# Performance work log

Measured on AMD Instinct MI355X. Metric: run time of the kernel, lower is better.

## Reference

```python
import jax, jax.numpy as jnp
import numpy as np

N = 50000      # nodes
F_IN = 500     # in_channels
MID = 64       # mid_layer_channel
H = 2          # heads
OUT = 40       # out_channels
E = 800000     # edges per order
ORDER = 3
NEG_SLOPE = 0.2


def _gat(x, edge_index, W, a_src, a_dst, b, concat):
    # PyG-style GATConv (eval mode, dropout off), with self loops.
    n = x.shape[0]
    heads, ch = a_src.shape
    h = (x @ W).reshape(n, heads, ch)                    # [N,H,C]
    loop = jnp.arange(n)
    src = jnp.concatenate([edge_index[0], loop])
    dst = jnp.concatenate([edge_index[1], loop])
    al_s = jnp.sum(h * a_src, axis=-1)                   # [N,H]
    al_d = jnp.sum(h * a_dst, axis=-1)                   # [N,H]
    e = jax.nn.leaky_relu(al_s[src] + al_d[dst], NEG_SLOPE)   # [Etot,H]
    m = jax.ops.segment_max(e, dst, num_segments=n)      # softmax over incoming edges per dst
    ex = jnp.exp(e - m[dst])
    den = jax.ops.segment_sum(ex, dst, num_segments=n)
    alpha = ex / (den[dst] + 1e-16)
    out = jax.ops.segment_sum(alpha[:, :, None] * h[src], dst, num_segments=n)  # [N,H,C]
    if concat:
        return out.reshape(n, heads * ch) + b
    return out.mean(axis=1) + b


def _aggr(states, Wmix, wfin):
    # NOrderAggrConv (depth=2): mix order states with [order,order] weights + ELU,
    # then reduce to a single state with a learned [order] combination.
    h = jnp.stack(states, axis=1)                        # [N,order,C]
    h = jax.nn.elu(jnp.einsum('nkc,kj->njc', h, Wmix))
    return jnp.einsum('nkc,k->nc', h, wfin)


def setup_inputs():
    key = jax.random.key(0)
    ks = jax.random.split(key, 40)
    d = {}
    d['node_feature'] = jax.random.normal(ks[0], (N, F_IN), jnp.float32)
    for o in range(ORDER):
        d[f'adj{o}'] = jax.random.randint(ks[1 + o], (2, E), 0, N)
    i = 4
    s = 0.05
    layer_dims = [(F_IN, MID, H * MID), (MID * H, OUT, OUT)]
    for l, (fin, c, bdim) in enumerate(layer_dims):
        for o in range(ORDER):
            d[f'W_{l}_{o}'] = jax.random.normal(ks[i], (fin, H * c), jnp.float32) * s; i += 1
            d[f'as_{l}_{o}'] = jax.random.normal(ks[i], (H, c), jnp.float32) * s; i += 1
            d[f'ad_{l}_{o}'] = jax.random.normal(ks[i], (H, c), jnp.float32) * s; i += 1
            d[f'b_{l}_{o}'] = jnp.zeros((bdim,), jnp.float32)
    for l in range(2):
        d[f'agg{l}_W'] = jax.random.normal(ks[i], (ORDER, ORDER), jnp.float32) * 0.5; i += 1
        d[f'agg{l}_w'] = jnp.full((ORDER,), 1.0 / ORDER, jnp.float32)
    return d


def reference(node_feature, adj0, adj1, adj2,
              W_0_0, as_0_0, ad_0_0, b_0_0,
              W_0_1, as_0_1, ad_0_1, b_0_1,
              W_0_2, as_0_2, ad_0_2, b_0_2,
              W_1_0, as_1_0, ad_1_0, b_1_0,
              W_1_1, as_1_1, ad_1_1, b_1_1,
              W_1_2, as_1_2, ad_1_2, b_1_2,
              agg0_W, agg0_w, agg1_W, agg1_w):
    adjs = (adj0, adj1, adj2)
    p0 = ((W_0_0, as_0_0, ad_0_0, b_0_0),
          (W_0_1, as_0_1, ad_0_1, b_0_1),
          (W_0_2, as_0_2, ad_0_2, b_0_2))
    p1 = ((W_1_0, as_1_0, ad_1_0, b_1_0),
          (W_1_1, as_1_1, ad_1_1, b_1_1),
          (W_1_2, as_1_2, ad_1_2, b_1_2))
    aggs = ((agg0_W, agg0_w), (agg1_W, agg1_w))
    x = node_feature  # eval mode: dropout is identity
    for l, params in enumerate((p0, p1)):
        concat = (l == 0)
        states = [jax.nn.elu(_gat(x, adjs[o], *params[o], concat)) for o in range(ORDER)]
        x = _aggr(states, *aggs[l])
    return jax.nn.log_softmax(x, axis=1)
```

## Files before the change

### kernel.cpp

```cpp
#include <hip/hip_runtime.h>
#include <cstdint>
#include <cstddef>
#include <math.h>


typedef __attribute__((ext_vector_type(8))) short short8;
typedef __attribute__((ext_vector_type(4))) float f32x4;
typedef __attribute__((ext_vector_type(2))) float f32x2;

struct P3f { const float* p[3]; };
struct P3c { const int* p[3]; };

__device__ __forceinline__ float leakyf(float x) { return x > 0.f ? x : 0.2f * x; }
__device__ __forceinline__ float eluf(float x)   { return x > 0.f ? x : expm1f(x); }

__device__ __forceinline__ unsigned short bf16r(float x) {
  unsigned int u = __float_as_uint(x);
  u += 0x7fffu + ((u >> 16) & 1u);
  return (unsigned short)(u >> 16);
}
__device__ __forceinline__ float bflo(unsigned int u) { return __uint_as_float(u << 16); }
__device__ __forceinline__ float bfhi(unsigned int u) { return __uint_as_float(u & 0xffff0000u); }

__device__ __forceinline__ void bf8_fma2(uint4 q, float xx, f32x2* a) {
  f32x2 v0 = {bflo(q.x), bfhi(q.x)};
  f32x2 v1 = {bflo(q.y), bfhi(q.y)};
  f32x2 v2 = {bflo(q.z), bfhi(q.z)};
  f32x2 v3 = {bflo(q.w), bfhi(q.w)};
  a[0] += xx * v0;
  a[1] += xx * v1;
  a[2] += xx * v2;
  a[3] += xx * v3;
}

__global__ __launch_bounds__(256) void zero_int_kernel(int* p, int n) {
  int i = blockIdx.x * blockDim.x + threadIdx.x;
  if (i < n) p[i] = 0;
}

__global__ __launch_bounds__(256) void convA_kernel(const float* __restrict__ A,
    unsigned short* __restrict__ Ab, int M, int K, int Kpad) {
  int i = blockIdx.x * blockDim.x + threadIdx.x;
  int row = i >> 6;
  int koff = (i & 63) * 8;
  if (row >= M) return;
  const float* ap = A + (size_t)row * K;
  unsigned short v[8];
  if (koff + 8 <= K) {
    float4 q0 = ((const float4*)(ap + koff))[0];
    float4 q1 = ((const float4*)(ap + koff))[1];
    v[0] = bf16r(q0.x); v[1] = bf16r(q0.y); v[2] = bf16r(q0.z); v[3] = bf16r(q0.w);
    v[4] = bf16r(q1.x); v[5] = bf16r(q1.y); v[6] = bf16r(q1.z); v[7] = bf16r(q1.w);
  } else {
#pragma unroll
    for (int k = 0; k < 8; ++k)
      v[k] = (koff + k < K) ? bf16r(ap[koff + k]) : (unsigned short)0;
  }
  *(uint4*)(Ab + (size_t)row * Kpad + koff) = *(const uint4*)v;
}

__global__ __launch_bounds__(256) void count3_kernel(P3c adj, int* __restrict__ cntb,
                                                     int E, int N) {
  int i = blockIdx.x * blockDim.x + threadIdx.x;
  int o = blockIdx.y;
  if (i < E) atomicAdd(&cntb[o * N + adj.p[o][E + i]], 1);
}

#define SCAN_T 256
#define SCAN_VPT 8
#define SCAN_TILE 2048

__global__ __launch_bounds__(SCAN_T) void scan1_kernel(const int* __restrict__ cntb,
    int* __restrict__ rowptrb, int* __restrict__ bsums, int N) {
  __shared__ int lds[SCAN_T];
  const int o = blockIdx.y;
  const int* cnt = cntb + o * N;
  int* rowptr = rowptrb + o * (N + 1);
  int t = threadIdx.x;
  int base = blockIdx.x * SCAN_TILE + t * SCAN_VPT;
  int v[SCAN_VPT];
  int s = 0;
#pragma unroll
  for (int i = 0; i < SCAN_VPT; ++i) {
    int idx = base + i;
    int x = (idx < N) ? cnt[idx] : 0;
    s += x;
    v[i] = s;
  }
  lds[t] = s;
  __syncthreads();
  for (int off = 1; off < SCAN_T; off <<= 1) {
    int add = (t >= off) ? lds[t - off] : 0;
    __syncthreads();
    lds[t] += add;
    __syncthreads();
  }
  int excl = (t > 0) ? lds[t - 1] : 0;
#pragma unroll
  for (int i = 0; i < SCAN_VPT; ++i) {
    int idx = base + i;
    if (idx < N) rowptr[idx + 1] = excl + v[i];
  }
  if (t == SCAN_T - 1) bsums[o * 64 + blockIdx.x] = lds[t];
}

__global__ void scan2_kernel(int* bsums, int nb, int* rowptrb, int N) {
  if (threadIdx.x == 0 && blockIdx.x == 0) {
    for (int o = 0; o < 3; ++o) {
      int run = 0;
      for (int i = 0; i < nb; ++i) {
        int x = bsums[o * 64 + i];
        bsums[o * 64 + i] = run;
        run += x;
      }
      rowptrb[o * (N + 1)] = 0;
    }
  }
}

__global__ __launch_bounds__(256) void scan3_kernel(int* __restrict__ rowptrb,
    const int* __restrict__ bsums, int N) {
  int idx = blockIdx.x * blockDim.x + threadIdx.x;
  int o = blockIdx.y;
  if (idx < N) rowptrb[o * (N + 1) + idx + 1] += bsums[o * 64 + idx / SCAN_TILE];
}

__global__ __launch_bounds__(256) void fill3_kernel(P3c adj,
    const int* __restrict__ rowptrb, int* __restrict__ curb,
    int* __restrict__ colvb, int E, int N) {
  int i = blockIdx.x * blockDim.x + threadIdx.x;
  int o = blockIdx.y;
  if (i < E) {
    const int* a = adj.p[o];
    int d = a[E + i];
    int pos = atomicAdd(&curb[o * N + d], 1);
    colvb[(size_t)o * E + rowptrb[o * (N + 1) + d] + pos] = a[i];
  }
}

__global__ __launch_bounds__(256) void conv_bt3_kernel(P3f W,
    unsigned short* __restrict__ BtB, int K, int NC, int Kpad) {
  int n = blockIdx.y;
  int o = blockIdx.z;
  int k = blockIdx.x * 256 + threadIdx.x;
  if (k >= Kpad) return;
  float v = (k < K) ? W.p[o][(size_t)k * NC + n] : 0.f;
  BtB[(size_t)o * NC * Kpad + (size_t)n * Kpad + k] = bf16r(v);
}

#define GBM 128
#define LDSTRIDE 40

template<int NT>
__global__ __launch_bounds__(256) void mfma_gemm_kernel(
    const unsigned short* __restrict__ Ab, const unsigned short* __restrict__ BtB,
    P3f asp, P3f adp, unsigned short* __restrict__ CbB,
    float2* __restrict__ alsB, float2* __restrict__ aldB, int M, int Kpad) {
  constexpr int NC = NT * 16;
  constexpr int CH = NT * 8;
  __shared__ unsigned short As[GBM * LDSTRIDE];
  __shared__ unsigned short Bs[NC * LDSTRIDE];
  const int t = threadIdx.x;
  const int o = blockIdx.y;
  const int wave = t >> 6, lane = t & 63;
  const int quad = lane >> 4, l16 = lane & 15;
  const int m0 = blockIdx.x * GBM;
  const unsigned short* Bt = BtB + (size_t)o * NC * Kpad;
  unsigned short* Cb = CbB + (size_t)o * M * NC;
  float2* al_s = alsB + (size_t)o * M;
  float2* al_d = aldB + (size_t)o * M;
  const float* a_src = asp.p[o];
  const float* a_dst = adp.p[o];

  f32x4 acc[2][NT];
#pragma unroll
  for (int i = 0; i < 2; ++i)
#pragma unroll
    for (int j = 0; j < NT; ++j) acc[i][j] = (f32x4){0.f, 0.f, 0.f, 0.f};

  const int arow = t >> 1;
  const int akoff = (t & 1) * 16;
  const int gm = m0 + arow;
  const unsigned short* arowp = Ab + (size_t)gm * Kpad;
  const unsigned short* browp = Bt + (size_t)arow * Kpad;

  for (int k0 = 0; k0 < Kpad; k0 += 32) {
    if (k0) __syncthreads();
    const int kb = k0 + akoff;
    {
      uint4 q0 = {0, 0, 0, 0}, q1 = {0, 0, 0, 0};
      if (gm < M) {
        const uint4* p = (const uint4*)(arowp + kb);
        q0 = p[0]; q1 = p[1];
      }
      short8* dst = (short8*)&As[arow * LDSTRIDE + akoff];
      union { uint4 q; short8 s; } c0, c1;
      c0.q = q0; c1.q = q1;
      dst[0] = c0.s;
      dst[1] = c1.s;
    }
    if (arow < NC) {
      const uint4* p = (const uint4*)(browp + kb);
      uint4 q0 = p[0], q1 = p[1];
      short8* dst = (short8*)&Bs[arow * LDSTRIDE + akoff];
      union { uint4 q; short8 s; } c0, c1;
      c0.q = q0; c1.q = q1;
      dst[0] = c0.s;
      dst[1] = c1.s;
    }
    __syncthreads();
    short8 af[2];
#pragma unroll
    for (int rt = 0; rt < 2; ++rt)
      af[rt] = *(const short8*)&As[(wave * 32 + rt * 16 + l16) * LDSTRIDE + quad * 8];
    short8 bfv[NT];
#pragma unroll
    for (int ct = 0; ct < NT; ++ct)
      bfv[ct] = *(const short8*)&Bs[(ct * 16 + l16) * LDSTRIDE + quad * 8];
#pragma unroll
    for (int rt = 0; rt < 2; ++rt)
#pragma unroll
      for (int ct = 0; ct < NT; ++ct)
        acc[rt][ct] = __builtin_amdgcn_mfma_f32_16x16x32_bf16(af[rt], bfv[ct],
                                                              acc[rt][ct], 0, 0, 0);
  }
  float asv[NT], adv[NT];
#pragma unroll
  for (int ct = 0; ct < NT; ++ct) {
    int col = ct * 16 + l16;
    asv[ct] = a_src[col];
    adv[ct] = a_dst[col];
  }
#pragma unroll
  for (int rt = 0; rt < 2; ++rt) {
    int gr0 = m0 + wave * 32 + rt * 16 + quad * 4;
#pragma unroll
    for (int r = 0; r < 4; ++r) {
      int gr = gr0 + r;
      float ps0 = 0.f, ps1 = 0.f, pd0 = 0.f, pd1 = 0.f;
#pragma unroll
      for (int ct = 0; ct < NT; ++ct) {
        int col = ct * 16 + l16;
        float v = acc[rt][ct][r];
        if (gr < M) Cb[(size_t)gr * NC + col] = bf16r(v);
        if (col < CH) { ps0 += v * asv[ct]; pd0 += v * adv[ct]; }
        else          { ps1 += v * asv[ct]; pd1 += v * adv[ct]; }
      }
#pragma unroll
      for (int off = 1; off < 16; off <<= 1) {
        ps0 += __shfl_xor(ps0, off, 64);
        ps1 += __shfl_xor(ps1, off, 64);
        pd0 += __shfl_xor(pd0, off, 64);
        pd1 += __shfl_xor(pd1, off, 64);
      }
      if (l16 == 0 && gr < M) {
        al_s[gr] = make_float2(ps0, ps1);
        al_d[gr] = make_float2(pd0, pd1);
      }
    }
  }
}

template<int C, int CONCAT>
__global__ __launch_bounds__(256) void gat_aggr4_kernel(
    const unsigned short* __restrict__ hB, const float2* __restrict__ alsB,
    const float2* __restrict__ aldB, const int* __restrict__ rowptrB,
    const int* __restrict__ colvB, P3f biasp, unsigned short* __restrict__ outB,
    int N, int E) {
  constexpr int HC = 2 * C;
  constexpr int FL = HC / 8;
  constexpr int ES = 64 / FL;
  constexpr int HB = C / 8;
  constexpr int OW = CONCAT ? HC : C;
  const int o = blockIdx.y;
  const unsigned short* h = hB + (size_t)o * N * HC;
  const float2* al_s = alsB + (size_t)o * N;
  const float2* al_d = aldB + (size_t)o * N;
  const int* rowptr = rowptrB + o * (N + 1);
  const float* bias = biasp.p[o];
  unsigned short* out = outB + (size_t)o * N * OW;

  int w = (blockIdx.x * blockDim.x + threadIdx.x) >> 6;
  int lane = threadIdx.x & 63;
  if (w >= N) return;
  const int eslot = lane / FL;
  const int f4 = lane - eslot * FL;
  const bool glane = lane < ES * FL;
  const float2 ad = al_d[w];
  const float2 asf = al_s[w];
  const int beg = rowptr[w], end = rowptr[w + 1];
  const int deg = end - beg;
  const int* colv = colvB + (size_t)o * E;

  const float xs0 = __expf(leakyf(asf.x + ad.x));
  const float xs1 = __expf(leakyf(asf.y + ad.y));

  f32x2 acc[4] = {}, acc2[4] = {};
  float dp0 = 0.f, dp1 = 0.f;

  auto gstep = [&](int s_reg, float x0_reg, float x1_reg, int j, int cnt, f32x2* a) {
    int sj = __shfl(s_reg, j, 64);
    float xa = __shfl(x0_reg, j, 64);
    float xb = __shfl(x1_reg, j, 64);
    if (glane && j < cnt) {
      uint4 q = ((const uint4*)(h + (size_t)sj * HC))[f4];
      bf8_fma2(q, (f4 < HB) ? xa : xb, a);
    }
  };

  if (deg <= 64) {
    int i = beg + lane;
    bool in = i < end;
    int s = in ? colv[i] : 0;
    float2 a = in ? al_s[s] : make_float2(0.f, 0.f);
    float x0 = in ? __expf(leakyf(a.x + ad.x)) : 0.f;
    float x1 = in ? __expf(leakyf(a.y + ad.y)) : 0.f;
    dp0 = x0; dp1 = x1;
    for (int jj = 0; jj < deg; jj += 4 * ES) {
      gstep(s, x0, x1, jj + eslot, deg, acc);
      gstep(s, x0, x1, jj + ES + eslot, deg, acc2);
      gstep(s, x0, x1, jj + 2 * ES + eslot, deg, acc);
      gstep(s, x0, x1, jj + 3 * ES + eslot, deg, acc2);
    }
  } else {
    for (int base = beg; base < end; base += 64) {
      int i = base + lane;
      bool in = i < end;
      int s = in ? colv[i] : 0;
      float2 a = in ? al_s[s] : make_float2(0.f, 0.f);
      float x0 = in ? __expf(leakyf(a.x + ad.x)) : 0.f;
      float x1 = in ? __expf(leakyf(a.y + ad.y)) : 0.f;
      dp0 += x0; dp1 += x1;
      int cnt = min(64, end - base);
      for (int jj = 0; jj < cnt; jj += 4 * ES) {
        gstep(s, x0, x1, jj + eslot, cnt, acc);
        gstep(s, x0, x1, jj + ES + eslot, cnt, acc2);
        gstep(s, x0, x1, jj + 2 * ES + eslot, cnt, acc);
        gstep(s, x0, x1, jj + 3 * ES + eslot, cnt, acc2);
      }
    }
  }

#pragma unroll
  for (int off = 1; off < 64; off <<= 1) {
    dp0 += __shfl_xor(dp0, off, 64);
    dp1 += __shfl_xor(dp1, off, 64);
  }
  float den0 = dp0 + xs0, den1 = dp1 + xs1;

  if (eslot == 0) {
    uint4 q = ((const uint4*)(h + (size_t)w * HC))[f4];
    bf8_fma2(q, (f4 < HB) ? xs0 : xs1, acc);
  }
#pragma unroll
  for (int i = 0; i < 4; ++i) acc[i] += acc2[i];

  auto fold = [&](int off, int lim) {
#pragma unroll
    for (int i = 0; i < 4; ++i) {
      float t0 = __shfl(acc[i][0], lane + off, 64);
      float t1 = __shfl(acc[i][1], lane + off, 64);
      if (lane < lim) { acc[i][0] += t0; acc[i][1] += t1; }
    }
  };
  if (ES == 4) {
    fold(2 * FL, 2 * FL);
    fold(FL, FL);
  } else {
    fold(3 * FL, 3 * FL);
    fold(FL, FL);
    fold(2 * FL, FL);
  }

  float inv0 = 1.f / (den0 + 1e-16f), inv1 = 1.f / (den1 + 1e-16f);
  if (CONCAT) {
    if (lane < FL) {
      float xx = (f4 < HB) ? inv0 : inv1;
      const float* bp = bias + f4 * 8;
      unsigned int pk[4];
#pragma unroll
      for (int i = 0; i < 4; ++i) {
        unsigned short lo = bf16r(eluf(acc[i][0] * xx + bp[2 * i]));
        unsigned short hi = bf16r(eluf(acc[i][1] * xx + bp[2 * i + 1]));
        pk[i] = (unsigned int)lo | ((unsigned int)hi << 16);
      }
      ((uint4*)(out + (size_t)w * OW + f4 * 8))[0] = make_uint4(pk[0], pk[1], pk[2], pk[3]);
    }
  } else {
    float p[8];
#pragma unroll
    for (int i = 0; i < 4; ++i) {
      p[2 * i]     = __shfl(acc[i][0], lane + HB, 64);
      p[2 * i + 1] = __shfl(acc[i][1], lane + HB, 64);
    }
    if (lane < HB) {
      const float* bp = bias + f4 * 8;
      unsigned int pk[4];
#pragma unroll
      for (int i = 0; i < 4; ++i) {
        float v0 = 0.5f * (acc[i][0] * inv0 + p[2 * i] * inv1) + bp[2 * i];
        float v1 = 0.5f * (acc[i][1] * inv0 + p[2 * i + 1] * inv1) + bp[2 * i + 1];
        pk[i] = (unsigned int)bf16r(eluf(v0)) | ((unsigned int)bf16r(eluf(v1)) << 16);
      }
      ((uint4*)(out + (size_t)w * OW + f4 * 8))[0] = make_uint4(pk[0], pk[1], pk[2], pk[3]);
    }
  }
}

template<int BF16OUT>
__global__ __launch_bounds__(256) void mixb_kernel(const unsigned short* __restrict__ sb,
    const float* __restrict__ Wm, const float* __restrict__ wf,
    void* __restrict__ out, int perU) {
  int i = blockIdx.x * blockDim.x + threadIdx.x;
  if (i >= perU) return;
  const unsigned int* sp = (const unsigned int*)sb;
  unsigned int u0 = sp[i];
  unsigned int u1 = sp[perU + i];
  unsigned int u2 = sp[2 * perU + i];
  float a0 = bflo(u0), a1 = bfhi(u0);
  float b0 = bflo(u1), b1 = bfhi(u1);
  float c0 = bflo(u2), c1 = bfhi(u2);
  float r0 = 0.f, r1 = 0.f;
#pragma unroll
  for (int j = 0; j < 3; ++j) {
    float w0 = Wm[j], w1 = Wm[3 + j], w2 = Wm[6 + j], wj = wf[j];
    r0 += wj * eluf(a0 * w0 + b0 * w1 + c0 * w2);
    r1 += wj * eluf(a1 * w0 + b1 * w1 + c1 * w2);
  }
  if (BF16OUT) {
    ((unsigned int*)out)[i] = (unsigned int)bf16r(r0) | ((unsigned int)bf16r(r1) << 16);
  } else {
    ((float2*)out)[i] = make_float2(r0, r1);
  }
}

__global__ __launch_bounds__(256) void log_softmax_kernel(const float* __restrict__ x,
    float* __restrict__ out, int N, int C) {
  int w = (blockIdx.x * blockDim.x + threadIdx.x) >> 6;
  int lane = threadIdx.x & 63;
  if (w >= N) return;
  float v = (lane < C) ? x[(size_t)w * C + lane] : -INFINITY;
  float mx = v;
#pragma unroll
  for (int off = 1; off < 64; off <<= 1) mx = fmaxf(mx, __shfl_xor(mx, off, 64));
  float ex = (lane < C) ? expf(v - mx) : 0.f;
  float s = ex;
#pragma unroll
  for (int off = 1; off < 64; off <<= 1) s += __shfl_xor(s, off, 64);
  if (lane < C) out[(size_t)w * C + lane] = v - mx - logf(s);
}

extern "C" void kernel_launch(void* const* d_in, const int* in_sizes, int n_in,
                              void* d_out, int out_size, void* d_ws, size_t ws_size,
                              hipStream_t stream) {
  const int F_IN = 500;
  const int N = in_sizes[0] / F_IN;
  const int E = in_sizes[1] / 2;
  const int HC0 = 128;
  const int HC1 = 80;
  const int C1 = 40;
  const int K0pad = 512, K1pad = 128;

  const float* x0 = (const float*)d_in[0];
  P3c adj;
  adj.p[0] = (const int*)d_in[1];
  adj.p[1] = (const int*)d_in[2];
  adj.p[2] = (const int*)d_in[3];
  P3f W0p, as0p, ad0p, b0p, W1p, as1p, ad1p, b1p;
  for (int o = 0; o < 3; ++o) {
    W0p.p[o]  = (const float*)d_in[4 + 4 * o + 0];
    as0p.p[o] = (const float*)d_in[4 + 4 * o + 1];
    ad0p.p[o] = (const float*)d_in[4 + 4 * o + 2];
    b0p.p[o]  = (const float*)d_in[4 + 4 * o + 3];
    W1p.p[o]  = (const float*)d_in[16 + 4 * o + 0];
    as1p.p[o] = (const float*)d_in[16 + 4 * o + 1];
    ad1p.p[o] = (const float*)d_in[16 + 4 * o + 2];
    b1p.p[o]  = (const float*)d_in[16 + 4 * o + 3];
  }
  const float* agg0W = (const float*)d_in[28];
  const float* agg0w = (const float*)d_in[29];
  const float* agg1W = (const float*)d_in[30];
  const float* agg1w = (const float*)d_in[31];

  char* ws = (char*)d_ws;
  size_t off = 0;
  auto alloc = [&](size_t bytes) -> void* {
    off = (off + 255) & ~(size_t)255;
    void* p = ws + off;
    off += bytes;
    return p;
  };
  int* rowptrb = (int*)alloc((size_t)3 * (N + 1) * 4);
  int* colvb   = (int*)alloc((size_t)3 * E * 4);
  int* cntcur  = (int*)alloc((size_t)6 * N * 4);
  int* bsums   = (int*)alloc(3 * 64 * 4);
  unsigned short* x0b = (unsigned short*)alloc((size_t)N * K0pad * 2);
  unsigned short* hB  = (unsigned short*)alloc((size_t)3 * N * HC0 * 2);
  unsigned short* stB = (unsigned short*)alloc((size_t)3 * N * HC0 * 2);
  float* x2 = (float*)alloc((size_t)N * C1 * 4);
  float2* alsB = (float2*)alloc((size_t)3 * N * 8);
  float2* aldB = (float2*)alloc((size_t)3 * N * 8);
  unsigned short* Bt0B = (unsigned short*)alloc((size_t)3 * HC0 * K0pad * 2);
  unsigned short* Bt1B = (unsigned short*)alloc((size_t)3 * HC1 * K1pad * 2);
  (void)ws_size;

  const int TB = 256;
  const int nbE = (E + TB - 1) / TB;
  const int nbN = (N + TB - 1) / TB;
  const int scanBlocks = (N + SCAN_TILE - 1) / SCAN_TILE;
  const int waveBlocks = (int)(((size_t)N * 64 + TB - 1) / TB);
  const int gemmBlocks = (N + GBM - 1) / GBM;

  convA_kernel<<<(int)(((size_t)N * 64 + TB - 1) / TB), TB, 0, stream>>>(
      x0, x0b, N, F_IN, K0pad);
  conv_bt3_kernel<<<dim3((K0pad + 255) / 256, HC0, 3), TB, 0, stream>>>(W0p, Bt0B, F_IN, HC0, K0pad);
  conv_bt3_kernel<<<dim3((K1pad + 255) / 256, HC1, 3), TB, 0, stream>>>(W1p, Bt1B, HC0, HC1, K1pad);

  zero_int_kernel<<<(6 * N + TB - 1) / TB, TB, 0, stream>>>(cntcur, 6 * N);
  count3_kernel<<<dim3(nbE, 3), TB, 0, stream>>>(adj, cntcur, E, N);
  scan1_kernel<<<dim3(scanBlocks, 3), SCAN_T, 0, stream>>>(cntcur, rowptrb, bsums, N);
  scan2_kernel<<<1, 64, 0, stream>>>(bsums, scanBlocks, rowptrb, N);
  scan3_kernel<<<dim3(nbN, 3), TB, 0, stream>>>(rowptrb, bsums, N);
  fill3_kernel<<<dim3(nbE, 3), TB, 0, stream>>>(adj, rowptrb, cntcur + 3 * N, colvb, E, N);

  mfma_gemm_kernel<8><<<dim3(gemmBlocks, 3), TB, 0, stream>>>(
      x0b, Bt0B, as0p, ad0p, hB, alsB, aldB, N, K0pad);
  gat_aggr4_kernel<64, 1><<<dim3(waveBlocks, 3), TB, 0, stream>>>(
      hB, alsB, aldB, rowptrb, colvb, b0p, stB, N, E);
  mixb_kernel<1><<<((N * HC0 / 2) + TB - 1) / TB, TB, 0, stream>>>(
      stB, agg0W, agg0w, stB, N * HC0 / 2);

  mfma_gemm_kernel<5><<<dim3(gemmBlocks, 3), TB, 0, stream>>>(
      stB, Bt1B, as1p, ad1p, hB, alsB, aldB, N, K1pad);
  gat_aggr4_kernel<40, 0><<<dim3(waveBlocks, 3), TB, 0, stream>>>(
      hB, alsB, aldB, rowptrb, colvb, b1p, stB, N, E);
  mixb_kernel<0><<<((N * C1 / 2) + TB - 1) / TB, TB, 0, stream>>>(
      stB, agg1W, agg1w, x2, N * C1 / 2);

  log_softmax_kernel<<<waveBlocks, TB, 0, stream>>>(x2, (float*)d_out, N, C1);
}
```

Before: 848.3 us.

## Restructure GAT aggregation to direct per-lane edge loads with permlane reductions

Each wave now works through a node's edges 16 at a time, with a fixed 4-edge-slot by 16-lane layout. Every lane loads its own column indices and source attention scores directly, replacing the earlier broadcast of a 64-edge batch through shuffles. Four gathers per iteration are issued before use to raise memory-level parallelism. The cross-slot and denominator reductions use permlane32/permlane16 swaps instead of generic shuffles, and the self-loop row is loaded early. In exchange, colv and al_s are loaded redundantly across lanes, and for C=40 lanes 10-15 of each slot sit idle.

Result: slower. 903.1 us (+6.5%).

```diff
diff --git a/kernel.cpp b/kernel.cpp
--- a/kernel.cpp
+++ b/kernel.cpp
@@ -7,6 +7,7 @@
 typedef __attribute__((ext_vector_type(8))) short short8;
 typedef __attribute__((ext_vector_type(4))) float f32x4;
 typedef __attribute__((ext_vector_type(2))) float f32x2;
+typedef unsigned int u32x2 __attribute__((ext_vector_type(2)));
 
 struct P3f { const float* p[3]; };
 struct P3c { const int* p[3]; };
@@ -21,6 +22,24 @@
 }
 __device__ __forceinline__ float bflo(unsigned int u) { return __uint_as_float(u << 16); }
 __device__ __forceinline__ float bfhi(unsigned int u) { return __uint_as_float(u & 0xffff0000u); }
+
+__device__ __forceinline__ float fold32v(float v) {
+#if __has_builtin(__builtin_amdgcn_permlane32_swap)
+  u32x2 r = __builtin_amdgcn_permlane32_swap(__float_as_uint(v), __float_as_uint(v), false, false);
+  return __uint_as_float(r[1]);
+#else
+  return __shfl_xor(v, 32, 64);
+#endif
+}
+__device__ __forceinline__ float fold16v(float v) {
+#if __has_builtin(__builtin_amdgcn_permlane16_swap)
+  u32x2 r = __builtin_amdgcn_permlane16_swap(__float_as_uint(v), __float_as_uint(v), false, false);
+  return __uint_as_float(r[1]);
+#else
+  return __uint_as_float((unsigned int)__builtin_amdgcn_ds_swizzle(
+      (int)__float_as_uint(v), 0x401F));
+#endif
+}
 
 __device__ __forceinline__ void bf8_fma2(uint4 q, float xx, f32x2* a) {
   f32x2 v0 = {bflo(q.x), bfhi(q.x)};
@@ -262,14 +281,13 @@
 }
 
 template<int C, int CONCAT>
-__global__ __launch_bounds__(256) void gat_aggr4_kernel(
+__global__ __launch_bounds__(256) void gat_direct_kernel(
     const unsigned short* __restrict__ hB, const float2* __restrict__ alsB,
     const float2* __restrict__ aldB, const int* __restrict__ rowptrB,
     const int* __restrict__ colvB, P3f biasp, unsigned short* __restrict__ outB,
     int N, int E) {
   constexpr int HC = 2 * C;
-  constexpr int FL = HC / 8;
-  constexpr int ES = 64 / FL;
+  constexpr int FLd = HC / 8;
   constexpr int HB = C / 8;
   constexpr int OW = CONCAT ? HC : C;
   const int o = blockIdx.y;
@@ -280,102 +298,92 @@
   const float* bias = biasp.p[o];
   unsigned short* out = outB + (size_t)o * N * OW;
 
-  int w = (blockIdx.x * blockDim.x + threadIdx.x) >> 6;
-  int lane = threadIdx.x & 63;
+  const int w = (blockIdx.x * blockDim.x + threadIdx.x) >> 6;
+  const int lane = threadIdx.x & 63;
   if (w >= N) return;
-  const int eslot = lane / FL;
-  const int f4 = lane - eslot * FL;
-  const bool glane = lane < ES * FL;
+  const int eslot = lane >> 4;
+  const int f4 = lane & 15;
+  const bool hl = f4 < FLd;
+
   const float2 ad = al_d[w];
   const float2 asf = al_s[w];
   const int beg = rowptr[w], end = rowptr[w + 1];
-  const int deg = end - beg;
   const int* colv = colvB + (size_t)o * E;
 
   const float xs0 = __expf(leakyf(asf.x + ad.x));
   const float xs1 = __expf(leakyf(asf.y + ad.y));
 
+  uint4 qself = make_uint4(0, 0, 0, 0);
+  if (lane < FLd) qself = ((const uint4*)(h + (size_t)w * HC))[f4];
+
   f32x2 acc[4] = {}, acc2[4] = {};
   float dp0 = 0.f, dp1 = 0.f;
 
-  auto gstep = [&](int s_reg, float x0_reg, float x1_reg, int j, int cnt, f32x2* a) {
-    int sj = __shfl(s_reg, j, 64);
-    float xa = __shfl(x0_reg, j, 64);
-    float xb = __shfl(x1_reg, j, 64);
-    if (glane && j < cnt) {
-      uint4 q = ((const uint4*)(h + (size_t)sj * HC))[f4];
-      bf8_fma2(q, (f4 < HB) ? xa : xb, a);
-    }
-  };
-
-  if (deg <= 64) {
-    int i = beg + lane;
-    bool in = i < end;
-    int s = in ? colv[i] : 0;
-    float2 a = in ? al_s[s] : make_float2(0.f, 0.f);
-    float x0 = in ? __expf(leakyf(a.x + ad.x)) : 0.f;
-    float x1 = in ? __expf(leakyf(a.y + ad.y)) : 0.f;
-    dp0 = x0; dp1 = x1;
-    for (int jj = 0; jj < deg; jj += 4 * ES) {
-      gstep(s, x0, x1, jj + eslot, deg, acc);
-      gstep(s, x0, x1, jj + ES + eslot, deg, acc2);
-      gstep(s, x0, x1, jj + 2 * ES + eslot, deg, acc);
-      gstep(s, x0, x1, jj + 3 * ES + eslot, deg, acc2);
-    }
-  } else {
-    for (int base = beg; base < end; base += 64) {
-      int i = base + lane;
-      bool in = i < end;
-      int s = in ? colv[i] : 0;
-      float2 a = in ? al_s[s] : make_float2(0.f, 0.f);
-      float x0 = in ? __expf(leakyf(a.x + ad.x)) : 0.f;
-      float x1 = in ? __expf(leakyf(a.y + ad.y)) : 0.f;
-      dp0 += x0; dp1 += x1;
-      int cnt = min(64, end - base);
-      for (int jj = 0; jj < cnt; jj += 4 * ES) {
-        gstep(s, x0, x1, jj + eslot, cnt, acc);
-        gstep(s, x0, x1, jj + ES + eslot, cnt, acc2);
-        gstep(s, x0, x1, jj + 2 * ES + eslot, cnt, acc);
-        gstep(s, x0, x1, jj + 3 * ES + eslot, cnt, acc2);
-      }
-    }
-  }
-
-#pragma unroll
-  for (int off = 1; off < 64; off <<= 1) {
-    dp0 += __shfl_xor(dp0, off, 64);
-    dp1 += __shfl_xor(dp1, off, 64);
-  }
-  float den0 = dp0 + xs0, den1 = dp1 + xs1;
-
-  if (eslot == 0) {
-    uint4 q = ((const uint4*)(h + (size_t)w * HC))[f4];
-    bf8_fma2(q, (f4 < HB) ? xs0 : xs1, acc);
-  }
+  for (int e0 = beg; e0 < end; e0 += 16) {
+    const int ea = e0 + eslot;
+    const int eb = ea + 4;
+    const int ec = ea + 8;
+    const int ed = ea + 12;
+    const bool va = ea < end, vb = eb < end, vc = ec < end, vd = ed < end;
+    const int sa = va ? colv[ea] : 0;
+    const int sb = vb ? colv[eb] : 0;
+    const int sc = vc ? colv[ec] : 0;
+    const int sd = vd ? colv[ed] : 0;
+    uint4 qa = make_uint4(0, 0, 0, 0), qb = qa, qc = qa, qd = qa;
+    if (hl) {
+      qa = ((const uint4*)(h + (size_t)sa * HC))[f4];
+      qb = ((const uint4*)(h + (size_t)sb * HC))[f4];
+      qc = ((const uint4*)(h + (size_t)sc * HC))[f4];
+      qd = ((const uint4*)(h + (size_t)sd * HC))[f4];
+    }
+    const float2 aa = al_s[sa];
+    const float2 ab = al_s[sb];
+    const float2 ac = al_s[sc];
+    const float2 adx = al_s[sd];
+    const float xa0 = va ? __expf(leakyf(aa.x + ad.x)) : 0.f;
+    const float xa1 = va ? __expf(leakyf(aa.y + ad.y)) : 0.f;
+    const float xb0 = vb ? __expf(leakyf(ab.x + ad.x)) : 0.f;
+    const float xb1 = vb ? __expf(leakyf(ab.y + ad.y)) : 0.f;
+    const float xc0 = vc ? __expf(leakyf(ac.x + ad.x)) : 0.f;
+    const float xc1 = vc ? __expf(leakyf(ac.y + ad.y)) : 0.f;
+    const float xd0 = vd ? __expf(leakyf(adx.x + ad.x)) : 0.f;
+    const float xd1 = vd ? __expf(leakyf(adx.y + ad.y)) : 0.f;
+    dp0 += (xa0 + xb0) + (xc0 + xd0);
+    dp1 += (xa1 + xb1) + (xc1 + xd1);
+    if (hl) {
+      bf8_fma2(qa, (f4 < HB) ? xa0 : xa1, acc);
+      bf8_fma2(qb, (f4 < HB) ? xb0 : xb1, acc2);
+      bf8_fma2(qc, (f4 < HB) ? xc0 : xc1, acc);
+      bf8_fma2(qd, (f4 < HB) ? xd0 : xd1, acc2);
+    }
+  }
+
 #pragma unroll
   for (int i = 0; i < 4; ++i) acc[i] += acc2[i];
 
-  auto fold = [&](int off, int lim) {
-#pragma unroll
-    for (int i = 0; i < 4; ++i) {
-      float t0 = __shfl(acc[i][0], lane + off, 64);
-      float t1 = __shfl(acc[i][1], lane + off, 64);
-      if (lane < lim) { acc[i][0] += t0; acc[i][1] += t1; }
-    }
-  };
-  if (ES == 4) {
-    fold(2 * FL, 2 * FL);
-    fold(FL, FL);
-  } else {
-    fold(3 * FL, 3 * FL);
-    fold(FL, FL);
-    fold(2 * FL, FL);
-  }
-
-  float inv0 = 1.f / (den0 + 1e-16f), inv1 = 1.f / (den1 + 1e-16f);
+#pragma unroll
+  for (int i = 0; i < 4; ++i) {
+    acc[i][0] += fold32v(acc[i][0]);
+    acc[i][1] += fold32v(acc[i][1]);
+  }
+  dp0 += fold32v(dp0);
+  dp1 += fold32v(dp1);
+#pragma unroll
+  for (int i = 0; i < 4; ++i) {
+    acc[i][0] += fold16v(acc[i][0]);
+    acc[i][1] += fold16v(acc[i][1]);
+  }
+  dp0 += fold16v(dp0);
+  dp1 += fold16v(dp1);
+
+  const float den0 = dp0 + xs0, den1 = dp1 + xs1;
+
+  if (lane < FLd) bf8_fma2(qself, (f4 < HB) ? xs0 : xs1, acc);
+
+  const float inv0 = 1.f / (den0 + 1e-16f), inv1 = 1.f / (den1 + 1e-16f);
   if (CONCAT) {
-    if (lane < FL) {
-      float xx = (f4 < HB) ? inv0 : inv1;
+    if (lane < FLd) {
+      const float xx = (f4 < HB) ? inv0 : inv1;
       const float* bp = bias + f4 * 8;
       unsigned int pk[4];
 #pragma unroll
@@ -525,14 +533,14 @@
 
   mfma_gemm_kernel<8><<<dim3(gemmBlocks, 3), TB, 0, stream>>>(
       x0b, Bt0B, as0p, ad0p, hB, alsB, aldB, N, K0pad);
-  gat_aggr4_kernel<64, 1><<<dim3(waveBlocks, 3), TB, 0, stream>>>(
+  gat_direct_kernel<64, 1><<<dim3(waveBlocks, 3), TB, 0, stream>>>(
       hB, alsB, aldB, rowptrb, colvb, b0p, stB, N, E);
   mixb_kernel<1><<<((N * HC0 / 2) + TB - 1) / TB, TB, 0, stream>>>(
       stB, agg0W, agg0w, stB, N * HC0 / 2);
 
   mfma_gemm_kernel<5><<<dim3(gemmBlocks, 3), TB, 0, stream>>>(
       stB, Bt1B, as1p, ad1p, hB, alsB, aldB, N, K1pad);
-  gat_aggr4_kernel<40, 0><<<dim3(waveBlocks, 3), TB, 0, stream>>>(
+  gat_direct_kernel<40, 0><<<dim3(waveBlocks, 3), TB, 0, stream>>>(
       hB, alsB, aldB, rowptrb, colvb, b1p, stB, N, E);
   mixb_kernel<0><<<((N * C1 / 2) + TB - 1) / TB, TB, 0, stream>>>(
       stB, agg1W, agg1w, x2, N * C1 / 2);
```
